# Kernel tuning notes

Measured on AMD Instinct MI355X. Metric: run time of the kernel, lower is better.

The kernel has to match this reference:

```python
import jax, jax.numpy as jnp
import numpy as np

TEMPERATURE = 0.07
EPS = 1e-8
LAMBDA_CONTRASTIVE = 0.3
AMBIGUOUS_THRESHOLD = 0.05
LABEL_SMOOTHING = 0.1

B, D, NUM_DIMS, NUM_PIECES = 4096, 256, 19, 1024


def setup_inputs() -> dict:
    key = jax.random.key(0)
    ks = jax.random.split(key, 7)
    return {
        "z_a": jax.random.normal(ks[0], (B, D), dtype=jnp.float32),
        "z_b": jax.random.normal(ks[1], (B, D), dtype=jnp.float32),
        "ranking_logits": jax.random.normal(ks[2], (B, NUM_DIMS), dtype=jnp.float32),
        "labels_a": jax.random.uniform(ks[3], (B, NUM_DIMS), dtype=jnp.float32),
        "labels_b": jax.random.uniform(ks[4], (B, NUM_DIMS), dtype=jnp.float32),
        "piece_ids_a": jax.random.randint(ks[5], (B,), 0, NUM_PIECES, dtype=jnp.int64 if jax.config.jax_enable_x64 else jnp.int32),
        "piece_ids_b": jax.random.randint(ks[6], (B,), 0, NUM_PIECES, dtype=jnp.int64 if jax.config.jax_enable_x64 else jnp.int32),
    }


def _infonce(embeddings, piece_ids, temperature=TEMPERATURE, eps=EPS):
    # embeddings [N, D], piece_ids [N]. Same-piece samples are positives.
    norm = jnp.sqrt(jnp.sum(embeddings * embeddings, axis=-1, keepdims=True))
    z = embeddings / jnp.maximum(norm, eps)  # F.normalize semantics
    sim = (z @ z.T) / temperature  # [N, N]
    n = sim.shape[0]
    eye = jnp.eye(n, dtype=bool)
    piece_mask = piece_ids[None, :] == piece_ids[:, None]
    pos_mask = piece_mask & ~eye
    neg_mask = (~piece_mask) & ~eye
    # row-wise max subtraction (detached in torch) is a no-op on the value since
    # (pos - logsumexp) is shift-invariant; compute stably via masked logsumexp.
    neg_inf = jnp.array(-jnp.inf, sim.dtype)
    neg_lse = jax.scipy.special.logsumexp(jnp.where(neg_mask, sim, neg_inf), axis=-1)  # [N]
    valid_anchor = pos_mask.any(axis=1) & neg_mask.any(axis=1)  # [N]
    pair_mask = pos_mask & valid_anchor[:, None]  # each positive of a valid anchor
    # per-positive term: logsumexp([pos_sim, negs_of_row]) - pos_sim
    lse = jnp.logaddexp(sim, neg_lse[:, None])  # [N, N]
    term = jnp.where(pair_mask, lse - sim, 0.0)
    count = jnp.sum(pair_mask)
    loss = jnp.sum(term) / jnp.maximum(count, 1)
    return jnp.where(count > 0, loss, 0.0)


def _ranking_loss(logits, labels_a, labels_b,
                  ambiguous_threshold=AMBIGUOUS_THRESHOLD,
                  label_smoothing=LABEL_SMOOTHING):
    label_diff = labels_a - labels_b
    targets = (label_diff > 0).astype(logits.dtype)
    non_ambiguous = jnp.abs(label_diff) >= ambiguous_threshold
    targets = targets * (1.0 - label_smoothing) + 0.5 * label_smoothing
    # BCE-with-logits, elementwise, mean over non-ambiguous entries
    bce = jnp.maximum(logits, 0.0) - logits * targets + jnp.log1p(jnp.exp(-jnp.abs(logits)))
    cnt = jnp.sum(non_ambiguous)
    loss = jnp.sum(jnp.where(non_ambiguous, bce, 0.0)) / jnp.maximum(cnt, 1)
    return jnp.where(cnt > 0, loss, 0.0)


def reference(z_a, z_b, ranking_logits, labels_a, labels_b, piece_ids_a, piece_ids_b):
    l_rank = _ranking_loss(ranking_logits, labels_a, labels_b)
    all_z = jnp.concatenate([z_a, z_b], axis=0)        # [2B, D]
    all_pieces = jnp.concatenate([piece_ids_a, piece_ids_b], axis=0)  # [2B]
    l_contrast = _infonce(all_z, all_pieces)
    total = l_rank + LAMBDA_CONTRASTIVE * l_contrast
    return (total, l_rank, l_contrast)
```

## Files before the change

kernel.cpp:

```cpp
#include <hip/hip_runtime.h>
#include <hip/hip_bf16.h>
#include <math.h>

#define NTOT 8192
#define HB   4096
#define DIM  256
#define RANK_N (4096*19)
#define NORM_BLOCKS (NTOT/4)
#define RANK_BLOCKS (RANK_N/256)
#define ZERO_BLOCKS 2
#define INV_T 14.285714285714286f
#define SHIFT 16.0f
#define C1 20.609592f
#define C2 23.083120f
#define MAXP  48
#define POST_BLOCKS (NTOT/256)

typedef __attribute__((ext_vector_type(8))) short bf16x8_t;
typedef __attribute__((ext_vector_type(4))) float f32x4_t;

__device__ __forceinline__ unsigned short f2bf(float f) {
  union { float fv; unsigned int u; } v; v.fv = f;
  unsigned int u = v.u;
  unsigned int r = u + 0x7FFFu + ((u >> 16) & 1u);
  return (unsigned short)(r >> 16);
}

__device__ __forceinline__ const float* zrow(const float* za, const float* zb, int g) {
  return g < HB ? za + (size_t)g * DIM : zb + (size_t)(g - HB) * DIM;
}
__device__ __forceinline__ int piece_of(const int* pa, const int* pb, int g) {
  return g < HB ? pa[g] : pb[g - HB];
}

__device__ __forceinline__ void gload_lds16(const unsigned short* g, unsigned short* l) {
  __builtin_amdgcn_global_load_lds(
      (const __attribute__((address_space(1))) unsigned int*)g,
      (__attribute__((address_space(3))) unsigned int*)l, 16, 0, 0);
}

__global__ void k_pre(const float* __restrict__ za, const float* __restrict__ zb,
                      const float* __restrict__ logits, const float* __restrict__ la,
                      const float* __restrict__ lb,
                      const int* __restrict__ pa, const int* __restrict__ pb,
                      unsigned short* __restrict__ zn, float* __restrict__ rank_part,
                      float* __restrict__ neg_s, int* __restrict__ posCount,
                      float* __restrict__ accf, int* __restrict__ done) {
  __shared__ float sred[8];
  int bid = blockIdx.x;
  int t = threadIdx.x;
  if (bid < NORM_BLOCKS) {
    int lane = t & 63, w = t >> 6;
    int row = bid * 4 + w;
    const float* src = zrow(za, zb, row);
    float4 v = *reinterpret_cast<const float4*>(src + lane * 4);
    float ss = v.x * v.x + v.y * v.y + v.z * v.z + v.w * v.w;
    for (int o = 32; o; o >>= 1) ss += __shfl_xor(ss, o, 64);
    float inv = 1.0f / fmaxf(sqrtf(ss), 1e-8f);
    ushort4 o;
    o.x = f2bf(v.x * inv); o.y = f2bf(v.y * inv);
    o.z = f2bf(v.z * inv); o.w = f2bf(v.w * inv);
    int phys = (((lane >> 1) ^ (row & 7)) << 3) + ((lane & 1) << 2);
    *reinterpret_cast<ushort4*>(zn + (size_t)row * DIM + phys) = o;
  } else if (bid < NORM_BLOCKS + RANK_BLOCKS) {
    int rb = bid - NORM_BLOCKS;
    int e = rb * 256 + t;
    float lsum = 0.f, lcnt = 0.f;
    float diff = la[e] - lb[e];
    if (fabsf(diff) >= 0.05f) {
      float x = logits[e];
      float tgt = diff > 0.f ? 0.95f : 0.05f;
      lsum = fmaxf(x, 0.f) - x * tgt + log1pf(__expf(-fabsf(x)));
      lcnt = 1.f;
    }
    for (int o = 32; o; o >>= 1) { lsum += __shfl_xor(lsum, o, 64); lcnt += __shfl_xor(lcnt, o, 64); }
    int w = t >> 6, lane = t & 63;
    if (lane == 0) { sred[w * 2] = lsum; sred[w * 2 + 1] = lcnt; }
    __syncthreads();
    if (t == 0) {
      float S = 0.f, C = 0.f;
      for (int i = 0; i < 4; ++i) { S += sred[i * 2]; C += sred[i * 2 + 1]; }
      rank_part[rb * 2] = S;
      rank_part[rb * 2 + 1] = C;
    }
  } else {
    int z = bid - NORM_BLOCKS - RANK_BLOCKS;
    if (z == 0) {
      for (int k = t; k < NTOT; k += 256) neg_s[k] = 0.f;
      if (t == 0) { accf[0] = 0.f; accf[1] = 0.f; accf[2] = 0.f; accf[3] = 0.f; *done = 0; }
    } else {
      for (int k = t; k < NTOT; k += 256) posCount[k] = 0;
    }
  }
}

__global__ __launch_bounds__(256, 4)
void k_gram(const unsigned short* __restrict__ zn,
            const int* __restrict__ pa, const int* __restrict__ pb,
            float* __restrict__ neg_s, int* __restrict__ posCount,
            float* __restrict__ pos_sims) {
  __shared__ unsigned short Bs[2][32 * 256];
  const int t = threadIdx.x;
  const int lane = t & 63;
  const int w = t >> 6;
  const int l15 = lane & 15;
  const int lg = lane >> 4;
  const int it = blockIdx.x >> 4;
  const int chunk = blockIdx.x & 15;
  const int ibase = it * 128;
  const int jbase0 = chunk * 512;

  bf16x8_t afrag[2][8];
#pragma unroll
  for (int mt = 0; mt < 2; ++mt) {
    int garow = ibase + w * 32 + mt * 16 + l15;
    const unsigned short* asrc = zn + (size_t)garow * DIM;
    int sw = garow & 7;
#pragma unroll
    for (int ks = 0; ks < 8; ++ks)
      afrag[mt][ks] = *reinterpret_cast<const bf16x8_t*>(asrc + (((lg + ks * 4) ^ sw) << 3));
  }

  int prow[8];
#pragma unroll
  for (int mt = 0; mt < 2; ++mt)
#pragma unroll
    for (int r = 0; r < 4; ++r)
      prow[mt * 4 + r] = piece_of(pa, pb, ibase + w * 32 + mt * 16 + lg * 4 + r);

  float s[8] = {0.f, 0.f, 0.f, 0.f, 0.f, 0.f, 0.f, 0.f};

  const int srow = w * 8 + (lane >> 5);
  const int scol = (lane & 31) * 8;

#define STAGE(buf, jt_)                                                        \
  {                                                                            \
    int jb_ = jbase0 + (jt_) * 32;                                             \
    const unsigned short* g0 = zn + (size_t)(jb_ + srow) * DIM + scol;         \
    unsigned short* l0 = &Bs[buf][w * 2048];                                   \
    _Pragma("unroll")                                                          \
    for (int i_ = 0; i_ < 4; ++i_)                                             \
      gload_lds16(g0 + (size_t)(2 * i_) * DIM, l0 + i_ * 512);                 \
  }

  STAGE(0, 0)
  __syncthreads();

  int cur = 0;
  for (int jt = 0; jt < 16; ++jt) {
    if (jt < 15) STAGE(cur ^ 1, jt + 1)
    const unsigned short* Bb = &Bs[cur][0];
#pragma unroll
    for (int ct = 0; ct < 2; ++ct) {
      int jj = jbase0 + jt * 32 + ct * 16 + l15;
      int pc = piece_of(pa, pb, jj);
      int brow = ct * 16 + l15;
      int bsw = brow & 7;
      const unsigned short* bbase = Bb + brow * 256;
      f32x4_t acc0 = {0.f, 0.f, 0.f, 0.f};
      f32x4_t acc1 = {0.f, 0.f, 0.f, 0.f};
#pragma unroll
      for (int ks = 0; ks < 8; ++ks) {
        bf16x8_t bfrag = *reinterpret_cast<const bf16x8_t*>(bbase + (((lg + ks * 4) ^ bsw) << 3));
        acc0 = __builtin_amdgcn_mfma_f32_16x16x32_bf16(afrag[0][ks], bfrag, acc0, 0, 0, 0);
        acc1 = __builtin_amdgcn_mfma_f32_16x16x32_bf16(afrag[1][ks], bfrag, acc1, 0, 0, 0);
      }
#pragma unroll
      for (int r = 0; r < 4; ++r) {
        int gi0 = ibase + w * 32 + lg * 4 + r;
        if (pc != prow[r]) {
          s[r] += exp2f(acc0[r] * C1 - C2);
        } else if (jj != gi0) {
          int slot = atomicAdd(&posCount[gi0], 1);
          if (slot < MAXP) pos_sims[(size_t)gi0 * MAXP + slot] = acc0[r] * INV_T;
        }
        int gi1 = gi0 + 16;
        if (pc != prow[4 + r]) {
          s[4 + r] += exp2f(acc1[r] * C1 - C2);
        } else if (jj != gi1) {
          int slot = atomicAdd(&posCount[gi1], 1);
          if (slot < MAXP) pos_sims[(size_t)gi1 * MAXP + slot] = acc1[r] * INV_T;
        }
      }
    }
    __syncthreads();
    cur ^= 1;
  }
#pragma unroll
  for (int q = 0; q < 8; ++q) {
    float v = s[q];
    v += __shfl_xor(v, 1, 64);
    v += __shfl_xor(v, 2, 64);
    v += __shfl_xor(v, 4, 64);
    v += __shfl_xor(v, 8, 64);
    if (l15 == 0)
      atomicAdd(&neg_s[ibase + w * 32 + (q >> 2) * 16 + lg * 4 + (q & 3)], v);
  }
#undef STAGE
}

__global__ void k_post(const float* __restrict__ neg_s,
                       const int* __restrict__ posCount, const float* __restrict__ pos_sims,
                       const float* __restrict__ rank_part,
                       float* __restrict__ accf, int* __restrict__ done,
                       float* __restrict__ out) {
  int t = threadIdx.x;
  int i = blockIdx.x * 256 + t;
  float lsum = 0.f, lcnt = 0.f;
  int posCnt = posCount[i];
  if (posCnt > 0 && posCnt < NTOT - 1) {
    float nlse = SHIFT + logf(neg_s[i]);
    int m = posCnt < MAXP ? posCnt : MAXP;
    for (int s = 0; s < m; ++s) {
      float x = nlse - pos_sims[(size_t)i * MAXP + s];
      lsum += fmaxf(x, 0.f) + log1pf(__expf(-fabsf(x)));
    }
    lcnt = (float)posCnt;
  }
  for (int o = 32; o; o >>= 1) { lsum += __shfl_xor(lsum, o, 64); lcnt += __shfl_xor(lcnt, o, 64); }
  __shared__ float sred[8];
  __shared__ int isLast;
  int w = t >> 6, lane = t & 63;
  if (lane == 0) { sred[w * 2] = lsum; sred[w * 2 + 1] = lcnt; }
  __syncthreads();
  if (t == 0) {
    float S = 0.f, C = 0.f;
    for (int k = 0; k < 4; ++k) { S += sred[k * 2]; C += sred[k * 2 + 1]; }
    atomicAdd(&accf[2], S);
    atomicAdd(&accf[3], C);
    __threadfence();
    int old = atomicAdd(done, 1);
    isLast = (old == POST_BLOCKS - 1);
  }
  __syncthreads();
  if (isLast) {
    __threadfence();
    float rs = 0.f, rc = 0.f;
    for (int rb = t; rb < RANK_BLOCKS; rb += 256) {
      rs += rank_part[rb * 2];
      rc += rank_part[rb * 2 + 1];
    }
    for (int o = 32; o; o >>= 1) { rs += __shfl_xor(rs, o, 64); rc += __shfl_xor(rc, o, 64); }
    if (lane == 0) { sred[w * 2] = rs; sred[w * 2 + 1] = rc; }
    __syncthreads();
    if (t == 0) {
      float RS = 0.f, RC = 0.f;
      for (int k = 0; k < 4; ++k) { RS += sred[k * 2]; RC += sred[k * 2 + 1]; }
      float ps = accf[2], pcn = accf[3];
      float l_rank = RC > 0.f ? RS / RC : 0.f;
      float l_con = pcn > 0.f ? ps / pcn : 0.f;
      out[0] = l_rank + 0.3f * l_con;
      out[1] = l_rank;
      out[2] = l_con;
    }
  }
}

extern "C" void kernel_launch(void* const* d_in, const int* in_sizes, int n_in,
                              void* d_out, int out_size, void* d_ws, size_t ws_size,
                              hipStream_t stream) {
  const float* za     = (const float*)d_in[0];
  const float* zb     = (const float*)d_in[1];
  const float* logits = (const float*)d_in[2];
  const float* la     = (const float*)d_in[3];
  const float* lb     = (const float*)d_in[4];
  const int*   pa     = (const int*)d_in[5];
  const int*   pb     = (const int*)d_in[6];
  float* out = (float*)d_out;

  float* wsf = (float*)d_ws;
  int*   wsi = (int*)d_ws;
  float* accf      = wsf;
  int*   done      = wsi + 4;
  float* rank_part = wsf + 8;
  float* neg_s     = wsf + 616;
  int*   posCount  = wsi + 8808;
  float* pos_sims  = wsf + 17000;
  unsigned short* zn = (unsigned short*)(wsf + 410216);

  k_pre<<<NORM_BLOCKS + RANK_BLOCKS + ZERO_BLOCKS, 256, 0, stream>>>(
      za, zb, logits, la, lb, pa, pb, zn, rank_part, neg_s, posCount, accf, done);
  k_gram<<<1024, 256, 0, stream>>>(zn, pa, pb, neg_s, posCount, pos_sims);
  k_post<<<POST_BLOCKS, 256, 0, stream>>>(neg_s, posCount, pos_sims, rank_part, accf, done, out);
}
```

Measured before the change: 160.5 us.

## Exploit Gram matrix symmetry to skip lower-triangle tiles

Each block now skips column tiles below the diagonal and, for strictly upper tiles, accumulates the negative-exp sums and positive sims for both the row and the mirrored column. This roughly halves the MFMA and exp work of the Gram kernel. In exchange it adds column reductions via shuffles plus extra atomics on neg_s and posCount, and it leaves the block workload unbalanced, since many blocks exit early while others do up to the full tile count.

```diff
diff --git a/kernel.cpp b/kernel.cpp
--- a/kernel.cpp
+++ b/kernel.cpp
@@ -110,6 +110,11 @@
   const int ibase = it * 128;
   const int jbase0 = chunk * 512;
 
+  const int jt0raw = 4 * it - 16 * chunk;
+  const int jt0 = jt0raw > 0 ? jt0raw : 0;
+  if (jt0 >= 16) return;
+  const int dthr = jt0raw + 4;
+
   bf16x8_t afrag[2][8];
 #pragma unroll
   for (int mt = 0; mt < 2; ++mt) {
@@ -143,12 +148,13 @@
       gload_lds16(g0 + (size_t)(2 * i_) * DIM, l0 + i_ * 512);                 \
   }
 
-  STAGE(0, 0)
+  STAGE(0, jt0)
   __syncthreads();
 
   int cur = 0;
-  for (int jt = 0; jt < 16; ++jt) {
+  for (int jt = jt0; jt < 16; ++jt) {
     if (jt < 15) STAGE(cur ^ 1, jt + 1)
+    const bool docol = (jt >= dthr);
     const unsigned short* Bb = &Bs[cur][0];
 #pragma unroll
     for (int ct = 0; ct < 2; ++ct) {
@@ -165,22 +171,44 @@
         acc0 = __builtin_amdgcn_mfma_f32_16x16x32_bf16(afrag[0][ks], bfrag, acc0, 0, 0, 0);
         acc1 = __builtin_amdgcn_mfma_f32_16x16x32_bf16(afrag[1][ks], bfrag, acc1, 0, 0, 0);
       }
+      float ecol = 0.f;
 #pragma unroll
       for (int r = 0; r < 4; ++r) {
         int gi0 = ibase + w * 32 + lg * 4 + r;
         if (pc != prow[r]) {
-          s[r] += exp2f(acc0[r] * C1 - C2);
+          float e = exp2f(acc0[r] * C1 - C2);
+          s[r] += e;
+          ecol += e;
+        } else if (docol) {
+          float sim = acc0[r] * INV_T;
+          int s0 = atomicAdd(&posCount[gi0], 1);
+          if (s0 < MAXP) pos_sims[(size_t)gi0 * MAXP + s0] = sim;
+          int s1 = atomicAdd(&posCount[jj], 1);
+          if (s1 < MAXP) pos_sims[(size_t)jj * MAXP + s1] = sim;
         } else if (jj != gi0) {
-          int slot = atomicAdd(&posCount[gi0], 1);
-          if (slot < MAXP) pos_sims[(size_t)gi0 * MAXP + slot] = acc0[r] * INV_T;
+          int s0 = atomicAdd(&posCount[gi0], 1);
+          if (s0 < MAXP) pos_sims[(size_t)gi0 * MAXP + s0] = acc0[r] * INV_T;
         }
         int gi1 = gi0 + 16;
         if (pc != prow[4 + r]) {
-          s[4 + r] += exp2f(acc1[r] * C1 - C2);
+          float e = exp2f(acc1[r] * C1 - C2);
+          s[4 + r] += e;
+          ecol += e;
+        } else if (docol) {
+          float sim = acc1[r] * INV_T;
+          int s0 = atomicAdd(&posCount[gi1], 1);
+          if (s0 < MAXP) pos_sims[(size_t)gi1 * MAXP + s0] = sim;
+          int s1 = atomicAdd(&posCount[jj], 1);
+          if (s1 < MAXP) pos_sims[(size_t)jj * MAXP + s1] = sim;
         } else if (jj != gi1) {
-          int slot = atomicAdd(&posCount[gi1], 1);
-          if (slot < MAXP) pos_sims[(size_t)gi1 * MAXP + slot] = acc1[r] * INV_T;
+          int s0 = atomicAdd(&posCount[gi1], 1);
+          if (s0 < MAXP) pos_sims[(size_t)gi1 * MAXP + s0] = acc1[r] * INV_T;
         }
+      }
+      if (docol) {
+        ecol += __shfl_xor(ecol, 16, 64);
+        ecol += __shfl_xor(ecol, 32, 64);
+        if (lane < 16) atomicAdd(&neg_s[jj], ecol);
       }
     }
     __syncthreads();
```

Result: slower. 186.0 us (+15.9%).
